# Performance work log

Measured on AMD Instinct MI355X. Metric: run time of the kernel, lower is better.

The kernel has to match this reference:

```python
import jax, jax.numpy as jnp
import numpy as np
from jax import lax

STRIDE = (1, 1)
PADDING = ((1, 1), (1, 1))  # padding=1 for 3x3 kernel -> same spatial size


def _conv_one(xi, wi, bi):
    # xi: [C_in, H, W], wi: [C_out, C_in, k, k], bi: [C_out]
    out = lax.conv_general_dilated(
        xi[None], wi, window_strides=STRIDE, padding=PADDING,
        dimension_numbers=('NCHW', 'OIHW', 'NCHW'))
    return out[0] + bi[:, None, None]


def setup_inputs() -> dict:
    key = jax.random.key(0)
    k1, k2, k3, k4 = jax.random.split(key, 4)
    B, C_in, H, W = 16, 64, 128, 128
    C_out, K, ks = 64, 5, 3
    x = jax.random.normal(k1, (B, C_in, H, W), dtype=jnp.float32)
    weights = jax.random.uniform(k2, (B, K), dtype=jnp.float32)  # attention over K kernels
    Wbank = jax.random.normal(k3, (K, C_out, C_in, ks, ks), dtype=jnp.float32)
    bbank = jax.random.normal(k4, (K, C_out), dtype=jnp.float32) * 0.1
    return {"x": x, "weights": weights, "Wbank": Wbank, "bbank": bbank}


def reference(x, weights, Wbank, bbank):
    # Per-sample aggregated kernels: [B, C_out, C_in, k, k]
    agg_w = jnp.einsum('bk,koihw->boihw', weights, Wbank)
    # Per-sample aggregated bias: [B, C_out]
    agg_b = weights @ bbank
    # Grouped conv with groups = batch, expressed as vmapped per-sample conv
    return jax.vmap(_conv_one)(x, agg_w, agg_b)
```

## Files before the change

kernel.cpp:

```cpp
#include <hip/hip_runtime.h>
#include <hip/hip_bf16.h>


typedef __attribute__((ext_vector_type(8))) __bf16 bf16x8;
typedef __attribute__((ext_vector_type(16))) float f32x16;
typedef __attribute__((ext_vector_type(4))) unsigned int u32x4;

#define NB 16
#define CI 64
#define CO 64
#define HH 128
#define WW 128
#define KBANK 5
#define ASTR 36864

__device__ __forceinline__ unsigned short f2bfu(float f) {
    __hip_bfloat16 h = __float2bfloat16(f);
    unsigned short s;
    __builtin_memcpy(&s, &h, 2);
    return s;
}

__global__ void prep_kernel(const float* __restrict__ weights,
                            const float* __restrict__ Wbank,
                            const float* __restrict__ bbank,
                            short* __restrict__ aggw,
                            float* __restrict__ aggb) {
    int idx = blockIdx.x * 256 + threadIdx.x;
    int b   = idx / ASTR;
    int rem = idx - b * ASTR;
    int j   = rem & 7;
    int co5 = (rem >> 3) & 31;
    int g   = (rem >> 8) & 1;
    int mk  = rem >> 9;
    int m   = mk / 36;
    int ks  = mk - m * 36;
    int co  = m * 32 + co5;
    int k   = ks * 16 + g * 8 + j;
    int tap = k >> 6;
    int ci  = k & 63;
    float s = 0.f;
#pragma unroll
    for (int kk = 0; kk < KBANK; ++kk)
        s += weights[b * KBANK + kk] * Wbank[((kk * CO + co) * CI + ci) * 9 + tap];
    aggw[idx] = (short)f2bfu(s);
    if (k == 0) {
        float sb = 0.f;
#pragma unroll
        for (int kk = 0; kk < KBANK; ++kk)
            sb += weights[b * KBANK + kk] * bbank[kk * CO + co];
        aggb[b * CO + co] = sb;
    }
}

__device__ __forceinline__ void load16(const float* __restrict__ xb, int r,
                                       int sw, int scg, float pv[16]) {
#pragma unroll
    for (int i = 0; i < 16; ++i)
        pv[i] = xb[((size_t)(scg * 16 + i) * HH + r) * WW + sw];
}

__device__ __forceinline__ void write16(short* __restrict__ slot, int sw, int scg,
                                        const float pv[16]) {
#pragma unroll
    for (int h = 0; h < 2; ++h) {
        unsigned u0 = (unsigned)f2bfu(pv[h * 8 + 0]) | ((unsigned)f2bfu(pv[h * 8 + 1]) << 16);
        unsigned u1 = (unsigned)f2bfu(pv[h * 8 + 2]) | ((unsigned)f2bfu(pv[h * 8 + 3]) << 16);
        unsigned u2 = (unsigned)f2bfu(pv[h * 8 + 4]) | ((unsigned)f2bfu(pv[h * 8 + 5]) << 16);
        unsigned u3 = (unsigned)f2bfu(pv[h * 8 + 6]) | ((unsigned)f2bfu(pv[h * 8 + 7]) << 16);
        *(u32x4*)&slot[((scg * 2 + h) * 130 + sw + 1) * 8] = u32x4{u0, u1, u2, u3};
    }
}

__global__ __launch_bounds__(512, 2) void conv_kernel(const float* __restrict__ x,
                                                      const short* __restrict__ aggw,
                                                      const float* __restrict__ aggb,
                                                      float* __restrict__ out) {
    __shared__ short ring[4][8][130][8];

    const int t   = threadIdx.x;
    const int lin = blockIdx.x;
    const int b     = (lin & 7) * 2 + ((lin >> 3) & 1);
    const int strip = lin >> 4;
    const int r0    = strip * 8;

    const int l  = t & 63;
    const int wv = t >> 6;
    const int m  = wv >> 2;
    const int nq = wv & 3;
    const int lm = l & 31;
    const int g  = l >> 5;

    const int sw  = t & 127;
    const int scg = t >> 7;

    const float* xb = x + (size_t)b * CI * HH * WW;
    const short* Ab = aggw + (size_t)b * ASTR + (size_t)m * 36 * 512;

    bf16x8 A[36];
#pragma unroll
    for (int ks = 0; ks < 36; ++ks)
        A[ks] = *(const bf16x8*)(Ab + ks * 512 + l * 8);

    float bias[16];
#pragma unroll
    for (int rg = 0; rg < 16; ++rg)
        bias[rg] = aggb[b * CO + m * 32 + (rg & 3) + 8 * (rg >> 2) + 4 * g];

    if (t < 64) {
        int slot = t >> 4, ch = (t >> 1) & 7, px = (t & 1) * 129;
        *(u32x4*)&ring[slot][ch][px][0] = u32x4{0u, 0u, 0u, 0u};
    }

    {
        float pv0[16] = {0,0,0,0,0,0,0,0,0,0,0,0,0,0,0,0};
        float pv1[16], pv2[16];
        if (r0 >= 1) load16(xb, r0 - 1, sw, scg, pv0);
        load16(xb, r0,     sw, scg, pv1);
        load16(xb, r0 + 1, sw, scg, pv2);
        write16(&ring[0][0][0][0], sw, scg, pv0);
        write16(&ring[1][0][0][0], sw, scg, pv1);
        write16(&ring[2][0][0][0], sw, scg, pv2);
    }
    __syncthreads();

    for (int ri = 0; ri < 8; ++ri) {
        const int r = r0 + ri;

        float pv[16] = {0,0,0,0,0,0,0,0,0,0,0,0,0,0,0,0};
        const bool stage = (ri < 7);
        if (stage && (r + 2 < 128)) load16(xb, r + 2, sw, scg, pv);

        const short* s0 = &ring[(ri    ) & 3][0][0][0];
        const short* s1 = &ring[(ri + 1) & 3][0][0][0];
        const short* s2 = &ring[(ri + 2) & 3][0][0][0];

        f32x16 acc = (f32x16)0.0f;
#pragma unroll
        for (int ks = 0; ks < 36; ++ks) {
            const int tap = ks >> 2, q = ks & 3;
            const int dy = tap / 3, dx = tap - dy * 3;
            const short* sb = (dy == 0) ? s0 : (dy == 1) ? s1 : s2;
            const int pix = nq * 32 + dx + lm;
            bf16x8 bv = *(const bf16x8*)&sb[((q * 2 + g) * 130 + pix) * 8];
            acc = __builtin_amdgcn_mfma_f32_32x32x16_bf16(A[ks], bv, acc, 0, 0, 0);
        }

        const int wc = nq * 32 + lm;
#pragma unroll
        for (int rg = 0; rg < 16; ++rg) {
            int co = m * 32 + (rg & 3) + 8 * (rg >> 2) + 4 * g;
            out[(((size_t)b * CO + co) * HH + r) * WW + wc] = acc[rg] + bias[rg];
        }

        if (stage) write16((short*)&ring[(ri + 3) & 3][0][0][0], sw, scg, pv);
        __syncthreads();
    }
}

extern "C" void kernel_launch(void* const* d_in, const int* in_sizes, int n_in,
                              void* d_out, int out_size, void* d_ws, size_t ws_size,
                              hipStream_t stream) {
    const float* x       = (const float*)d_in[0];
    const float* weights = (const float*)d_in[1];
    const float* Wbank   = (const float*)d_in[2];
    const float* bbank   = (const float*)d_in[3];
    float* out = (float*)d_out;

    short* aggw = (short*)d_ws;
    float* aggb = (float*)((char*)d_ws + 1179648);

    prep_kernel<<<dim3((NB * ASTR) / 256), dim3(256), 0, stream>>>(weights, Wbank, bbank, aggw, aggb);
    conv_kernel<<<dim3(256), dim3(512), 0, stream>>>(x, aggw, aggb, out);
}
```

Before: 40.94 us.

## Split conv rows into two 64-pixel halves with halo columns, doubling block count

Each block now handles a 64-pixel-wide half of an 8-row strip, with 256 threads instead of 512, so the grid grows to 512 blocks and covers more CUs. Halo columns on both sides are loaded explicitly into a narrower shared ring. The row loop is fully unrolled, the MFMA loop is raised to a higher wave priority, and __syncthreads is replaced by an explicit lgkmcnt wait plus s_barrier. In exchange, each block reloads its A fragments and adds halo loads, and both halves of a row reread the same weights.

```diff
diff --git a/kernel.cpp b/kernel.cpp
--- a/kernel.cpp
+++ b/kernel.cpp
@@ -54,45 +54,58 @@
 }
 
 __device__ __forceinline__ void load16(const float* __restrict__ xb, int r,
-                                       int sw, int scg, float pv[16]) {
+                                       int w, int scg, float (&pv)[16]) {
 #pragma unroll
     for (int i = 0; i < 16; ++i)
-        pv[i] = xb[((size_t)(scg * 16 + i) * HH + r) * WW + sw];
+        pv[i] = xb[((size_t)(scg * 16 + i) * HH + r) * WW + w];
+}
+
+__device__ __forceinline__ void zero16(float (&pv)[16]) {
+#pragma unroll
+    for (int i = 0; i < 16; ++i) pv[i] = 0.f;
 }
 
 __device__ __forceinline__ void write16(short* __restrict__ slot, int sw, int scg,
-                                        const float pv[16]) {
+                                        const float (&pv)[16]) {
 #pragma unroll
     for (int h = 0; h < 2; ++h) {
         unsigned u0 = (unsigned)f2bfu(pv[h * 8 + 0]) | ((unsigned)f2bfu(pv[h * 8 + 1]) << 16);
         unsigned u1 = (unsigned)f2bfu(pv[h * 8 + 2]) | ((unsigned)f2bfu(pv[h * 8 + 3]) << 16);
         unsigned u2 = (unsigned)f2bfu(pv[h * 8 + 4]) | ((unsigned)f2bfu(pv[h * 8 + 5]) << 16);
         unsigned u3 = (unsigned)f2bfu(pv[h * 8 + 6]) | ((unsigned)f2bfu(pv[h * 8 + 7]) << 16);
-        *(u32x4*)&slot[((scg * 2 + h) * 130 + sw + 1) * 8] = u32x4{u0, u1, u2, u3};
+        *(u32x4*)&slot[((scg * 2 + h) * 66 + sw + 1) * 8] = u32x4{u0, u1, u2, u3};
     }
 }
 
-__global__ __launch_bounds__(512, 2) void conv_kernel(const float* __restrict__ x,
+__global__ __launch_bounds__(256, 2) void conv_kernel(const float* __restrict__ x,
                                                       const short* __restrict__ aggw,
                                                       const float* __restrict__ aggb,
                                                       float* __restrict__ out) {
-    __shared__ short ring[4][8][130][8];
+    __shared__ short bring[4][8][66][8];
 
     const int t   = threadIdx.x;
     const int lin = blockIdx.x;
-    const int b     = (lin & 7) * 2 + ((lin >> 3) & 1);
-    const int strip = lin >> 4;
-    const int r0    = strip * 8;
+    const int b   = (lin & 7) * 2 + ((lin >> 3) & 1);
+    const int sp  = lin >> 4;
+    const int strip = sp >> 1;
+    const int P   = (sp & 1) * 64;
+    const int r0  = strip * 8;
 
     const int l  = t & 63;
     const int wv = t >> 6;
-    const int m  = wv >> 2;
-    const int nq = wv & 3;
+    const int m  = wv >> 1;
+    const int np = wv & 1;
     const int lm = l & 31;
     const int g  = l >> 5;
 
-    const int sw  = t & 127;
-    const int scg = t >> 7;
+    const int sw  = t & 63;
+    const int scg = t >> 6;
+
+    const int hside = t >> 6;
+    const int hci   = t & 63;
+    const int hw    = P + (hside ? 64 : -1);
+    const int hpixl = hside ? 65 : 0;
+    const bool hvalid_w = ((unsigned)hw < 128u);
 
     const float* xb = x + (size_t)b * CI * HH * WW;
     const short* Ab = aggw + (size_t)b * ASTR + (size_t)m * 36 * 512;
@@ -107,54 +120,62 @@
     for (int rg = 0; rg < 16; ++rg)
         bias[rg] = aggb[b * CO + m * 32 + (rg & 3) + 8 * (rg >> 2) + 4 * g];
 
-    if (t < 64) {
-        int slot = t >> 4, ch = (t >> 1) & 7, px = (t & 1) * 129;
-        *(u32x4*)&ring[slot][ch][px][0] = u32x4{0u, 0u, 0u, 0u};
+#pragma unroll
+    for (int pr = 0; pr < 3; ++pr) {
+        const int r = r0 - 1 + pr;
+        const bool rv = ((unsigned)r < 128u);
+        float pv[16];
+        float hval = 0.f;
+        if (rv) load16(xb, r, P + sw, scg, pv); else zero16(pv);
+        if (t < 128 && rv && hvalid_w)
+            hval = xb[((size_t)hci * HH + r) * WW + hw];
+        write16(&bring[pr][0][0][0], sw, scg, pv);
+        if (t < 128)
+            bring[pr][hci >> 3][hpixl][hci & 7] = (short)f2bfu(hval);
     }
+    asm volatile("s_waitcnt lgkmcnt(0)" ::: "memory");
+    __builtin_amdgcn_s_barrier();
+    __builtin_amdgcn_sched_barrier(0);
 
-    {
-        float pv0[16] = {0,0,0,0,0,0,0,0,0,0,0,0,0,0,0,0};
-        float pv1[16], pv2[16];
-        if (r0 >= 1) load16(xb, r0 - 1, sw, scg, pv0);
-        load16(xb, r0,     sw, scg, pv1);
-        load16(xb, r0 + 1, sw, scg, pv2);
-        write16(&ring[0][0][0][0], sw, scg, pv0);
-        write16(&ring[1][0][0][0], sw, scg, pv1);
-        write16(&ring[2][0][0][0], sw, scg, pv2);
-    }
-    __syncthreads();
+#pragma unroll
+    for (int s = 0; s < 8; ++s) {
+        const int r = r0 + s;
 
-    for (int ri = 0; ri < 8; ++ri) {
-        const int r = r0 + ri;
-
-        float pv[16] = {0,0,0,0,0,0,0,0,0,0,0,0,0,0,0,0};
-        const bool stage = (ri < 7);
-        if (stage && (r + 2 < 128)) load16(xb, r + 2, sw, scg, pv);
-
-        const short* s0 = &ring[(ri    ) & 3][0][0][0];
-        const short* s1 = &ring[(ri + 1) & 3][0][0][0];
-        const short* s2 = &ring[(ri + 2) & 3][0][0][0];
+        float pv[16];
+        float hval = 0.f;
+        const int rn = r + 2;
+        const bool rv = (rn < 128);
+        if (rv) load16(xb, rn, P + sw, scg, pv); else zero16(pv);
+        if (t < 128 && rv && hvalid_w)
+            hval = xb[((size_t)hci * HH + rn) * WW + hw];
 
         f32x16 acc = (f32x16)0.0f;
+        __builtin_amdgcn_s_setprio(1);
 #pragma unroll
         for (int ks = 0; ks < 36; ++ks) {
             const int tap = ks >> 2, q = ks & 3;
             const int dy = tap / 3, dx = tap - dy * 3;
-            const short* sb = (dy == 0) ? s0 : (dy == 1) ? s1 : s2;
-            const int pix = nq * 32 + dx + lm;
-            bf16x8 bv = *(const bf16x8*)&sb[((q * 2 + g) * 130 + pix) * 8];
+            const short* sb = &bring[(s + dy) & 3][0][0][0];
+            const int pixl = np * 32 + lm + dx;
+            bf16x8 bv = *(const bf16x8*)&sb[((q * 2 + g) * 66 + pixl) * 8];
             acc = __builtin_amdgcn_mfma_f32_32x32x16_bf16(A[ks], bv, acc, 0, 0, 0);
         }
+        __builtin_amdgcn_s_setprio(0);
 
-        const int wc = nq * 32 + lm;
+        const int wc = P + np * 32 + lm;
 #pragma unroll
         for (int rg = 0; rg < 16; ++rg) {
             int co = m * 32 + (rg & 3) + 8 * (rg >> 2) + 4 * g;
             out[(((size_t)b * CO + co) * HH + r) * WW + wc] = acc[rg] + bias[rg];
         }
 
-        if (stage) write16((short*)&ring[(ri + 3) & 3][0][0][0], sw, scg, pv);
-        __syncthreads();
+        write16(&bring[(s + 3) & 3][0][0][0], sw, scg, pv);
+        if (t < 128)
+            bring[(s + 3) & 3][hci >> 3][hpixl][hci & 7] = (short)f2bfu(hval);
+
+        asm volatile("s_waitcnt lgkmcnt(0)" ::: "memory");
+        __builtin_amdgcn_s_barrier();
+        __builtin_amdgcn_sched_barrier(0);
     }
 }
 
@@ -171,5 +192,5 @@
     float* aggb = (float*)((char*)d_ws + 1179648);
 
     prep_kernel<<<dim3((NB * ASTR) / 256), dim3(256), 0, stream>>>(weights, Wbank, bbank, aggw, aggb);
-    conv_kernel<<<dim3(256), dim3(512), 0, stream>>>(x, aggw, aggb, out);
+    conv_kernel<<<dim3(512), dim3(256), 0, stream>>>(x, aggw, aggb, out);
 }
```

After: 71.28 us. 74.1% more time.
